# Performance work log

Hardware: AMD Instinct MI355X
Metric: run time of the kernel (lower is better)

Reference implementation:

```python
import jax, jax.numpy as jnp
import numpy as np

BATCH, N_MACS_PREV, CMS_PREV, NEUR_PREV = 256, 512, 8, 16
FILTER_LEN = 256
NUM_CMS, NUM_NEURONS = 32, 32
NUM_INPUTS = FILTER_LEN * CMS_PREV * NEUR_PREV  # 32768


def setup_inputs() -> dict:
    key = jax.random.key(0)
    k1, k2, k3 = jax.random.split(key, 3)
    x = jax.random.uniform(k1, (BATCH, N_MACS_PREV, CMS_PREV, NEUR_PREV), dtype=jnp.float32)
    input_filter = jax.random.randint(k2, (FILTER_LEN,), 0, N_MACS_PREV)
    # binary {0,1} weights, matching torch.randint(0, 2, ..., dtype=float32)
    weights = jax.random.randint(k3, (NUM_CMS, NUM_INPUTS, NUM_NEURONS), 0, 2).astype(jnp.float32)
    return {"x": x, "input_filter": input_filter, "weights": weights}


def reference(x, input_filter, weights):
    B = x.shape[0]
    # gather receptive field MACs and flatten: (B, num_inputs)
    xg = jnp.take(x, input_filter, axis=1).reshape(B, -1)
    # sum-normalize, nan_to_num handles all-zero rows (0/0 -> 0)
    xn = jnp.nan_to_num(xg / jnp.sum(xg, axis=-1, keepdims=True))
    # batched matmul: (B,I) x (C,I,N) -> (B,C,N)  (torch does (C,B,N) then permutes)
    acts = jnp.einsum('bi,cin->bcn', xn, weights)
    # familiarity-based softmax temperature
    familiarities = jnp.max(acts, axis=-1)          # (B, C)
    avg_fam = jnp.mean(familiarities)               # scalar
    softmax_temp = 1.0 / (avg_fam + 1e-4) - 1.0
    logits = acts / softmax_temp
    # categorical sample per (batch, cm); fixed key for determinism
    samples = jax.random.categorical(jax.random.key(42), logits, axis=-1)  # (B, C)
    # scatter one-hot write-out, int output as in torch
    out = jax.nn.one_hot(samples, NUM_NEURONS, dtype=jnp.int32)  # (B, C, N)
    return out
```

## Files before the change

kernel.cpp:

```cpp
#include <hip/hip_runtime.h>
#include <stdint.h>

#define BATCH 256
#define NMAC  512
#define ROWF  128
#define I_    32768
#define C_    32
#define N_    32
#define XROW  (NMAC * ROWF)

typedef float  f32x4  __attribute__((ext_vector_type(4)));
typedef __bf16 bf16x8 __attribute__((ext_vector_type(8)));

__device__ __forceinline__ uint32_t f2bf_rne(float f) {
    uint32_t u = __builtin_bit_cast(uint32_t, f);
    return (u + 0x7FFFu + ((u >> 16) & 1u)) >> 16;
}

__global__ __launch_bounds__(256) void k_sum(const float* __restrict__ x,
                                             const int* __restrict__ filt,
                                             float* __restrict__ S) {
    const int b = blockIdx.x;
    const int t = threadIdx.x;
    const float* xb = x + (size_t)b * XROW;
    float s = 0.f;
    for (int it = 0; it < 32; ++it) {
        int idx4 = it * 256 + t;
        int f = idx4 >> 5;
        int j4 = idx4 & 31;
        float4 v = *(const float4*)(xb + (size_t)filt[f] * ROWF + j4 * 4);
        s += v.x + v.y + v.z + v.w;
    }
    for (int o = 32; o > 0; o >>= 1) s += __shfl_down(s, o, 64);
    __shared__ float red[4];
    if ((t & 63) == 0) red[t >> 6] = s;
    __syncthreads();
    if (t == 0) S[b] = red[0] + red[1] + red[2] + red[3];
}

__global__ __launch_bounds__(256, 2) void k_gemm(const float* __restrict__ x,
                                                 const int* __restrict__ filt,
                                                 const float* __restrict__ w,
                                                 float* __restrict__ raw) {
    __shared__ __align__(16) unsigned short afr[32 * 512];
    __shared__ __align__(16) unsigned short wfr[8 * 512];

    const int t  = threadIdx.x;
    const int l  = t & 63;
    const int wv = t >> 6;
    const int chunk = blockIdx.x & 63;
    const int c0 = (blockIdx.x >> 6) * 4;

    f32x4 acc[4][8];
#pragma unroll
    for (int bt = 0; bt < 4; ++bt)
#pragma unroll
        for (int ct = 0; ct < 8; ++ct) acc[bt][ct] = f32x4{0.f, 0.f, 0.f, 0.f};

    const int ar     = t >> 3;
    const int ai     = t & 7;
    const int a_quad = ai >> 1;
    const int a_j    = (ai & 1) * 4;
    const int wn = t & 31;
    const int wc = t >> 5;

    for (int st = 0; st < 16; ++st) {
        const int ifull = chunk * 512 + st * 32;
        const int fidx  = filt[ifull >> 7];
        const int ioff  = ifull & 127;
        const float* xs = x + (size_t)fidx * ROWF + ioff;

#pragma unroll
        for (int rr = 0; rr < 8; ++rr) {
            int row = rr * 32 + ar;
            float4 v = *(const float4*)(xs + (size_t)row * XROW + ai * 4);
            uint32_t u0 = __builtin_bit_cast(uint32_t, v.x);
            uint32_t u1 = __builtin_bit_cast(uint32_t, v.y);
            uint32_t u2 = __builtin_bit_cast(uint32_t, v.z);
            uint32_t u3 = __builtin_bit_cast(uint32_t, v.w);
            float l0 = v.x - __builtin_bit_cast(float, u0 & 0xFFFF0000u);
            float l1 = v.y - __builtin_bit_cast(float, u1 & 0xFFFF0000u);
            float l2 = v.z - __builtin_bit_cast(float, u2 & 0xFFFF0000u);
            float l3 = v.w - __builtin_bit_cast(float, u3 & 0xFFFF0000u);
            uint2 hp, lp;
            hp.x = (u0 >> 16) | (u1 & 0xFFFF0000u);
            hp.y = (u2 >> 16) | (u3 & 0xFFFF0000u);
            lp.x = f2bf_rne(l0) | (f2bf_rne(l1) << 16);
            lp.y = f2bf_rne(l2) | (f2bf_rne(l3) << 16);
            int rt   = row >> 4;
            int lane = a_quad * 16 + (row & 15);
            int base = (rt * 2) * 512 + lane * 8 + a_j;
            *(uint2*)&afr[base]       = hp;
            *(uint2*)&afr[base + 512] = lp;
        }

#pragma unroll
        for (int q = 0; q < 8; ++q) {
            int sl  = wc + 8 * q;
            int c   = sl >> 4;
            int il  = (sl & 15) * 2;
            const float* wp = w + ((size_t)(c0 + c) * I_ + ifull + il) * N_ + wn;
            uint32_t u0 = __builtin_bit_cast(uint32_t, wp[0]);
            uint32_t u1 = __builtin_bit_cast(uint32_t, wp[N_]);
            uint32_t pk = (u0 >> 16) | (u1 & 0xFFFF0000u);
            int lane = (il >> 3) * 16 + (wn & 15);
            int ct   = c * 2 + (wn >> 4);
            *(uint32_t*)&wfr[ct * 512 + lane * 8 + (il & 7)] = pk;
        }
        __syncthreads();

        bf16x8 av[4][2];
#pragma unroll
        for (int bt = 0; bt < 4; ++bt)
#pragma unroll
            for (int p = 0; p < 2; ++p)
                av[bt][p] = *(const bf16x8*)&afr[((wv * 4 + bt) * 2 + p) * 512 + l * 8];
        bf16x8 bv[8];
#pragma unroll
        for (int ct = 0; ct < 8; ++ct)
            bv[ct] = *(const bf16x8*)&wfr[ct * 512 + l * 8];
#pragma unroll
        for (int bt = 0; bt < 4; ++bt)
#pragma unroll
            for (int ct = 0; ct < 8; ++ct) {
                acc[bt][ct] = __builtin_amdgcn_mfma_f32_16x16x32_bf16(av[bt][0], bv[ct], acc[bt][ct], 0, 0, 0);
                acc[bt][ct] = __builtin_amdgcn_mfma_f32_16x16x32_bf16(av[bt][1], bv[ct], acc[bt][ct], 0, 0, 0);
            }
        __syncthreads();
    }

    const int quad = l >> 4, n15 = l & 15;
#pragma unroll
    for (int bt = 0; bt < 4; ++bt) {
#pragma unroll
        for (int ct = 0; ct < 8; ++ct) {
            int c = c0 + (ct >> 1);
            int n = (ct & 1) * 16 + n15;
#pragma unroll
            for (int r = 0; r < 4; ++r) {
                int b = (wv * 4 + bt) * 16 + quad * 4 + r;
                atomicAdd(&raw[((size_t)b * C_ + c) * N_ + n], acc[bt][ct][r]);
            }
        }
    }
}

__global__ __launch_bounds__(256) void k_fam(const float* __restrict__ raw,
                                             const float* __restrict__ S,
                                             float* __restrict__ fam) {
    int r = blockIdx.x * 256 + threadIdx.x;
    const float4* ap = (const float4*)(raw + (size_t)r * N_);
    float m = -3.0e38f;
#pragma unroll
    for (int q = 0; q < 8; ++q) {
        float4 v = ap[q];
        m = fmaxf(m, fmaxf(fmaxf(v.x, v.y), fmaxf(v.z, v.w)));
    }
    m = m / S[r >> 5];
    for (int o = 32; o > 0; o >>= 1) m += __shfl_down(m, o, 64);
    __shared__ float red[4];
    if ((threadIdx.x & 63) == 0) red[threadIdx.x >> 6] = m;
    __syncthreads();
    if (threadIdx.x == 0) atomicAdd(fam, red[0] + red[1] + red[2] + red[3]);
}

__device__ __forceinline__ uint32_t rotl32(uint32_t x, uint32_t r) {
    return (x << r) | (x >> (32u - r));
}
__device__ __forceinline__ void threefry(uint32_t k0, uint32_t k1,
                                         uint32_t x0, uint32_t x1,
                                         uint32_t& o0, uint32_t& o1) {
    uint32_t ks2 = k0 ^ k1 ^ 0x1BD11BDAu;
    x0 += k0; x1 += k1;
    x0 += x1; x1 = rotl32(x1, 13); x1 ^= x0;
    x0 += x1; x1 = rotl32(x1, 15); x1 ^= x0;
    x0 += x1; x1 = rotl32(x1, 26); x1 ^= x0;
    x0 += x1; x1 = rotl32(x1, 6);  x1 ^= x0;
    x0 += k1; x1 += ks2 + 1u;
    x0 += x1; x1 = rotl32(x1, 17); x1 ^= x0;
    x0 += x1; x1 = rotl32(x1, 29); x1 ^= x0;
    x0 += x1; x1 = rotl32(x1, 16); x1 ^= x0;
    x0 += x1; x1 = rotl32(x1, 24); x1 ^= x0;
    x0 += ks2; x1 += k0 + 2u;
    x0 += x1; x1 = rotl32(x1, 13); x1 ^= x0;
    x0 += x1; x1 = rotl32(x1, 15); x1 ^= x0;
    x0 += x1; x1 = rotl32(x1, 26); x1 ^= x0;
    x0 += x1; x1 = rotl32(x1, 6);  x1 ^= x0;
    x0 += k0; x1 += k1 + 3u;
    x0 += x1; x1 = rotl32(x1, 17); x1 ^= x0;
    x0 += x1; x1 = rotl32(x1, 29); x1 ^= x0;
    x0 += x1; x1 = rotl32(x1, 16); x1 ^= x0;
    x0 += x1; x1 = rotl32(x1, 24); x1 ^= x0;
    x0 += k1; x1 += ks2 + 4u;
    x0 += x1; x1 = rotl32(x1, 13); x1 ^= x0;
    x0 += x1; x1 = rotl32(x1, 15); x1 ^= x0;
    x0 += x1; x1 = rotl32(x1, 26); x1 ^= x0;
    x0 += x1; x1 = rotl32(x1, 6);  x1 ^= x0;
    x0 += ks2; x1 += k0 + 5u;
    o0 = x0; o1 = x1;
}

__device__ __forceinline__ float gumbel_of(uint32_t bits) {
    uint32_t fb = (bits >> 9) | 0x3F800000u;
    float f = __builtin_bit_cast(float, fb) - 1.0f;
    float u = f + 1.17549435e-38f;
    return -logf(-logf(u));
}

__global__ __launch_bounds__(256) void k_sample(const float* __restrict__ raw,
                                                const float* __restrict__ S,
                                                const float* __restrict__ fam,
                                                int* __restrict__ out) {
    int r0 = blockIdx.x * 256 + threadIdx.x;
    int r1 = r0 + 4096;
    float avg  = fam[0] * (1.0f / 8192.0f);
    float temp = 1.0f / (avg + 1e-4f) - 1.0f;
    float sA = S[r0 >> 5], sB = S[r1 >> 5];
    const float* apA = raw + (size_t)r0 * N_;
    const float* apB = raw + (size_t)r1 * N_;

    float bestA = -3.4e38f, bestB = -3.4e38f;
    int biA = 0, biB = 0;
    for (int n = 0; n < 32; ++n) {
        uint32_t iA = (uint32_t)(r0 * 32 + n);
        uint32_t iB = (uint32_t)(r1 * 32 + n);
        uint32_t a0, a1, b0, b1;
        threefry(0u, 42u, 0u, iA, a0, a1);
        threefry(0u, 42u, 0u, iB, b0, b1);
        float vA = (apA[n] / sA) / temp + gumbel_of(a0 ^ a1);
        float vB = (apB[n] / sB) / temp + gumbel_of(b0 ^ b1);
        if (vA > bestA) { bestA = vA; biA = n; }
        if (vB > bestB) { bestB = vB; biB = n; }
    }
    int4* opA = (int4*)(out + (size_t)r0 * N_);
    int4* opB = (int4*)(out + (size_t)r1 * N_);
#pragma unroll
    for (int q = 0; q < 8; ++q) {
        int4 a, b;
        a.x = (q * 4 + 0) == biA; a.y = (q * 4 + 1) == biA;
        a.z = (q * 4 + 2) == biA; a.w = (q * 4 + 3) == biA;
        b.x = (q * 4 + 0) == biB; b.y = (q * 4 + 1) == biB;
        b.z = (q * 4 + 2) == biB; b.w = (q * 4 + 3) == biB;
        opA[q] = a; opB[q] = b;
    }
}

extern "C" void kernel_launch(void* const* d_in, const int* in_sizes, int n_in,
                              void* d_out, int out_size, void* d_ws, size_t ws_size,
                              hipStream_t stream) {
    const float* x    = (const float*)d_in[0];
    const int*   filt = (const int*)d_in[1];
    const float* w    = (const float*)d_in[2];
    int* out = (int*)d_out;

    char* ws = (char*)d_ws;
    float* raw = (float*)ws;
    float* fam = (float*)(ws + (1 << 20));
    float* S   = (float*)(ws + (1 << 20) + 128);

    hipMemsetAsync(ws, 0, (1 << 20) + 128, stream);
    hipLaunchKernelGGL(k_sum,    dim3(256), dim3(256), 0, stream, x, filt, S);
    hipLaunchKernelGGL(k_gemm,   dim3(512), dim3(256), 0, stream, x, filt, w, raw);
    hipLaunchKernelGGL(k_fam,    dim3(32),  dim3(256), 0, stream, raw, S, fam);
    hipLaunchKernelGGL(k_sample, dim3(16),  dim3(256), 0, stream, raw, S, fam, out);
}
```

Measured before the change: 305.8 us.

## Double-buffer GEMM loads, widen blocks to 512 threads, swizzle LDS, replace atomics with partial reduction

The split-K GEMM kernel now uses 512 threads per block, with each wave owning two row tiles. Global loads for the next K-step are prefetched into registers while the current step runs its MFMAs, and an XOR swizzle is applied to the LDS fragment layout to reduce bank conflicts. When the workspace is large enough, per-chunk partial results are written with plain stores and summed by a new reduction kernel, replacing the float atomics. This adds 64 partial buffers of traffic (about 32 MB) and one extra launch, and it raises register pressure from the prefetch buffers.

New measurement: 390.8 us. 1.28x slower.

```diff
diff --git a/kernel.cpp b/kernel.cpp
--- a/kernel.cpp
+++ b/kernel.cpp
@@ -8,6 +8,8 @@
 #define C_    32
 #define N_    32
 #define XROW  (NMAC * ROWF)
+#define NCH   64
+#define NST   16
 
 typedef float  f32x4  __attribute__((ext_vector_type(4)));
 typedef __bf16 bf16x8 __attribute__((ext_vector_type(8)));
@@ -38,10 +40,12 @@
     if (t == 0) S[b] = red[0] + red[1] + red[2] + red[3];
 }
 
-__global__ __launch_bounds__(256, 2) void k_gemm(const float* __restrict__ x,
+__global__ __launch_bounds__(512, 4) void k_gemm(const float* __restrict__ x,
                                                  const int* __restrict__ filt,
                                                  const float* __restrict__ w,
-                                                 float* __restrict__ raw) {
+                                                 float* __restrict__ part,
+                                                 float* __restrict__ raw,
+                                                 int use_part) {
     __shared__ __align__(16) unsigned short afr[32 * 512];
     __shared__ __align__(16) unsigned short wfr[8 * 512];
 
@@ -51,29 +55,68 @@
     const int chunk = blockIdx.x & 63;
     const int c0 = (blockIdx.x >> 6) * 4;
 
-    f32x4 acc[4][8];
-#pragma unroll
-    for (int bt = 0; bt < 4; ++bt)
-#pragma unroll
-        for (int ct = 0; ct < 8; ++ct) acc[bt][ct] = f32x4{0.f, 0.f, 0.f, 0.f};
-
-    const int ar     = t >> 3;
-    const int ai     = t & 7;
-    const int a_quad = ai >> 1;
-    const int a_j    = (ai & 1) * 4;
-    const int wn = t & 31;
-    const int wc = t >> 5;
-
-    for (int st = 0; st < 16; ++st) {
+    const int arow = t >> 1;
+    const int akq  = t & 1;
+    const int r15  = arow & 15;
+    const int rt_a = arow >> 4;
+    const float* xr = x + (size_t)arow * XROW + akq * 4;
+
+    const int wn  = t & 31;
+    const int wsl = t >> 5;
+
+    f32x4 acc0[8], acc1[8];
+#pragma unroll
+    for (int i = 0; i < 8; ++i) {
+        acc0[i] = f32x4{0.f, 0.f, 0.f, 0.f};
+        acc1[i] = f32x4{0.f, 0.f, 0.f, 0.f};
+    }
+
+    auto loadA = [&](int st, float4* A) {
         const int ifull = chunk * 512 + st * 32;
         const int fidx  = filt[ifull >> 7];
-        const int ioff  = ifull & 127;
-        const float* xs = x + (size_t)fidx * ROWF + ioff;
-
-#pragma unroll
-        for (int rr = 0; rr < 8; ++rr) {
-            int row = rr * 32 + ar;
-            float4 v = *(const float4*)(xs + (size_t)row * XROW + ai * 4);
+        const float* pa = xr + (size_t)fidx * ROWF + (ifull & 127);
+#pragma unroll
+        for (int jj = 0; jj < 4; ++jj)
+            A[jj] = *(const float4*)(pa + jj * 8);
+    };
+
+    auto loadW = [&](int st, uint2* W) {
+        const int ifull = chunk * 512 + st * 32;
+#pragma unroll
+        for (int q = 0; q < 2; ++q) {
+            int sl = wsl + 16 * q;
+            int c  = sl >> 3;
+            int kk = (sl & 7) * 4;
+            const float* wp = w + ((size_t)(c0 + c) * I_ + ifull + kk) * N_ + wn;
+            uint32_t u0 = __builtin_bit_cast(uint32_t, wp[0]);
+            uint32_t u1 = __builtin_bit_cast(uint32_t, wp[N_]);
+            uint32_t u2 = __builtin_bit_cast(uint32_t, wp[2 * N_]);
+            uint32_t u3 = __builtin_bit_cast(uint32_t, wp[3 * N_]);
+            W[q].x = (u0 >> 16) | (u1 & 0xFFFF0000u);
+            W[q].y = (u2 >> 16) | (u3 & 0xFFFF0000u);
+        }
+    };
+
+    auto storeW = [&](const uint2* W) {
+#pragma unroll
+        for (int q = 0; q < 2; ++q) {
+            int sl = wsl + 16 * q;
+            int c  = sl >> 3;
+            int kk = (sl & 7) * 4;
+            int L  = ((kk >> 3) << 4) + (wn & 15);
+            int P  = L ^ ((L >> 3) & 7);
+            int ct = c * 2 + (wn >> 4);
+            *(uint2*)&wfr[ct * 512 + P * 8 + (kk & 4)] = W[q];
+        }
+    };
+
+    auto storeA = [&](const float4* A) {
+#pragma unroll
+        for (int jj = 0; jj < 4; ++jj) {
+            float4 v = A[jj];
+            int k0 = (akq + 2 * jj) * 4;
+            int L  = ((k0 >> 3) << 4) + r15;
+            int P  = L ^ ((L >> 3) & 7);
             uint32_t u0 = __builtin_bit_cast(uint32_t, v.x);
             uint32_t u1 = __builtin_bit_cast(uint32_t, v.y);
             uint32_t u2 = __builtin_bit_cast(uint32_t, v.z);
@@ -87,62 +130,73 @@
             hp.y = (u2 >> 16) | (u3 & 0xFFFF0000u);
             lp.x = f2bf_rne(l0) | (f2bf_rne(l1) << 16);
             lp.y = f2bf_rne(l2) | (f2bf_rne(l3) << 16);
-            int rt   = row >> 4;
-            int lane = a_quad * 16 + (row & 15);
-            int base = (rt * 2) * 512 + lane * 8 + a_j;
+            int base = (rt_a * 2) * 512 + P * 8 + (k0 & 4);
             *(uint2*)&afr[base]       = hp;
             *(uint2*)&afr[base + 512] = lp;
         }
-
-#pragma unroll
-        for (int q = 0; q < 8; ++q) {
-            int sl  = wc + 8 * q;
-            int c   = sl >> 4;
-            int il  = (sl & 15) * 2;
-            const float* wp = w + ((size_t)(c0 + c) * I_ + ifull + il) * N_ + wn;
-            uint32_t u0 = __builtin_bit_cast(uint32_t, wp[0]);
-            uint32_t u1 = __builtin_bit_cast(uint32_t, wp[N_]);
-            uint32_t pk = (u0 >> 16) | (u1 & 0xFFFF0000u);
-            int lane = (il >> 3) * 16 + (wn & 15);
-            int ct   = c * 2 + (wn >> 4);
-            *(uint32_t*)&wfr[ct * 512 + lane * 8 + (il & 7)] = pk;
-        }
+    };
+
+    const int Pl8 = (l ^ ((l >> 3) & 7)) * 8;
+    auto MM = [&]() {
+        const int rt0 = wv * 2, rt1 = rt0 + 1;
+        bf16x8 a00 = *(const bf16x8*)&afr[(rt0 * 2 + 0) * 512 + Pl8];
+        bf16x8 a01 = *(const bf16x8*)&afr[(rt0 * 2 + 1) * 512 + Pl8];
+        bf16x8 a10 = *(const bf16x8*)&afr[(rt1 * 2 + 0) * 512 + Pl8];
+        bf16x8 a11 = *(const bf16x8*)&afr[(rt1 * 2 + 1) * 512 + Pl8];
+#pragma unroll
+        for (int i = 0; i < 8; ++i) {
+            bf16x8 b = *(const bf16x8*)&wfr[i * 512 + Pl8];
+            acc0[i] = __builtin_amdgcn_mfma_f32_16x16x32_bf16(a00, b, acc0[i], 0, 0, 0);
+            acc0[i] = __builtin_amdgcn_mfma_f32_16x16x32_bf16(a01, b, acc0[i], 0, 0, 0);
+            acc1[i] = __builtin_amdgcn_mfma_f32_16x16x32_bf16(a10, b, acc1[i], 0, 0, 0);
+            acc1[i] = __builtin_amdgcn_mfma_f32_16x16x32_bf16(a11, b, acc1[i], 0, 0, 0);
+        }
+    };
+
+    float4 Aa[4], Ab[4];
+    uint2  Wa[2], Wb[2];
+    loadA(0, Aa); loadW(0, Wa);
+    for (int st = 0; st < NST; st += 2) {
+        if (st) __syncthreads();
+        storeA(Aa); storeW(Wa);
+        loadA(st + 1, Ab); loadW(st + 1, Wb);
         __syncthreads();
-
-        bf16x8 av[4][2];
-#pragma unroll
-        for (int bt = 0; bt < 4; ++bt)
-#pragma unroll
-            for (int p = 0; p < 2; ++p)
-                av[bt][p] = *(const bf16x8*)&afr[((wv * 4 + bt) * 2 + p) * 512 + l * 8];
-        bf16x8 bv[8];
-#pragma unroll
-        for (int ct = 0; ct < 8; ++ct)
-            bv[ct] = *(const bf16x8*)&wfr[ct * 512 + l * 8];
-#pragma unroll
-        for (int bt = 0; bt < 4; ++bt)
-#pragma unroll
-            for (int ct = 0; ct < 8; ++ct) {
-                acc[bt][ct] = __builtin_amdgcn_mfma_f32_16x16x32_bf16(av[bt][0], bv[ct], acc[bt][ct], 0, 0, 0);
-                acc[bt][ct] = __builtin_amdgcn_mfma_f32_16x16x32_bf16(av[bt][1], bv[ct], acc[bt][ct], 0, 0, 0);
+        MM();
+        __syncthreads();
+        storeA(Ab); storeW(Wb);
+        if (st + 2 < NST) { loadA(st + 2, Aa); loadW(st + 2, Wa); }
+        __syncthreads();
+        MM();
+    }
+
+    const int quad = l >> 4, n15 = l & 15;
+    float* dst = use_part ? (part + (size_t)chunk * (BATCH * C_ * N_)) : raw;
+#pragma unroll
+    for (int rr = 0; rr < 2; ++rr) {
+        const f32x4* ac = rr ? acc1 : acc0;
+        const int bbase = (wv * 2 + rr) * 16 + quad * 4;
+#pragma unroll
+        for (int i = 0; i < 8; ++i) {
+            int c = c0 + (i >> 1);
+            int n = (i & 1) * 16 + n15;
+#pragma unroll
+            for (int r = 0; r < 4; ++r) {
+                size_t idx = ((size_t)(bbase + r) * C_ + c) * N_ + n;
+                if (use_part) dst[idx] = ac[i][r];
+                else          atomicAdd(&dst[idx], ac[i][r]);
             }
-        __syncthreads();
-    }
-
-    const int quad = l >> 4, n15 = l & 15;
-#pragma unroll
-    for (int bt = 0; bt < 4; ++bt) {
-#pragma unroll
-        for (int ct = 0; ct < 8; ++ct) {
-            int c = c0 + (ct >> 1);
-            int n = (ct & 1) * 16 + n15;
-#pragma unroll
-            for (int r = 0; r < 4; ++r) {
-                int b = (wv * 4 + bt) * 16 + quad * 4 + r;
-                atomicAdd(&raw[((size_t)b * C_ + c) * N_ + n], acc[bt][ct][r]);
-            }
-        }
-    }
+        }
+    }
+}
+
+__global__ __launch_bounds__(256) void k_reduce(const float* __restrict__ part,
+                                                float* __restrict__ raw) {
+    const int i4 = blockIdx.x * 256 + threadIdx.x;
+    const f32x4* p = (const f32x4*)part;
+    f32x4 s = f32x4{0.f, 0.f, 0.f, 0.f};
+#pragma unroll 8
+    for (int ch = 0; ch < NCH; ++ch) s += p[(size_t)ch * 65536 + i4];
+    ((f32x4*)raw)[i4] = s;
 }
 
 __global__ __launch_bounds__(256) void k_fam(const float* __restrict__ raw,
@@ -254,13 +308,23 @@
     int* out = (int*)d_out;
 
     char* ws = (char*)d_ws;
-    float* raw = (float*)ws;
-    float* fam = (float*)(ws + (1 << 20));
-    float* S   = (float*)(ws + (1 << 20) + 128);
-
-    hipMemsetAsync(ws, 0, (1 << 20) + 128, stream);
+    float* raw  = (float*)ws;
+    float* fam  = (float*)(ws + (1 << 20));
+    float* S    = (float*)(ws + (1 << 20) + 128);
+    float* part = (float*)(ws + (2u << 20));
+
+    const size_t need = (2u << 20) + (size_t)NCH * (BATCH * C_ * N_) * sizeof(float);
+    const int use_part = (ws_size >= need) ? 1 : 0;
+
+    if (use_part) {
+        hipMemsetAsync(ws + (1 << 20), 0, 128, stream);
+    } else {
+        hipMemsetAsync(ws, 0, (1 << 20) + 128, stream);
+    }
     hipLaunchKernelGGL(k_sum,    dim3(256), dim3(256), 0, stream, x, filt, S);
-    hipLaunchKernelGGL(k_gemm,   dim3(512), dim3(256), 0, stream, x, filt, w, raw);
+    hipLaunchKernelGGL(k_gemm,   dim3(512), dim3(512), 0, stream, x, filt, w, part, raw, use_part);
+    if (use_part)
+        hipLaunchKernelGGL(k_reduce, dim3(256), dim3(256), 0, stream, part, raw);
     hipLaunchKernelGGL(k_fam,    dim3(32),  dim3(256), 0, stream, raw, S, fam);
     hipLaunchKernelGGL(k_sample, dim3(16),  dim3(256), 0, stream, raw, S, fam, out);
 }
```

## Replace GEMM split-K atomics with partial buffers and a fused reduce kernel

Applied to the files above, without the earlier changes.

Each split-K chunk of the GEMM now writes its partial (B,C,N) tile to its own slice of a workspace buffer instead of issuing float atomicAdds into a shared output. A new reduce kernel sums the 64 partials, writes the raw activations, and computes the familiarity max and global sum, replacing the separate k_fam kernel. The goal is to remove heavy atomic contention (64 adds per output element). The cost is about 64 MB of extra global writes and reads. The new path runs only when the workspace holds at least about 66 MB; otherwise the old atomic path is used.

Result: faster. 280.7 us (-8.2%).

```diff
diff --git a/kernel.cpp b/kernel.cpp
--- a/kernel.cpp
+++ b/kernel.cpp
@@ -8,6 +8,7 @@
 #define C_    32
 #define N_    32
 #define XROW  (NMAC * ROWF)
+#define NCH   64
 
 typedef float  f32x4  __attribute__((ext_vector_type(4)));
 typedef __bf16 bf16x8 __attribute__((ext_vector_type(8)));
@@ -41,7 +42,9 @@
 __global__ __launch_bounds__(256, 2) void k_gemm(const float* __restrict__ x,
                                                  const int* __restrict__ filt,
                                                  const float* __restrict__ w,
-                                                 float* __restrict__ raw) {
+                                                 float* __restrict__ part,
+                                                 float* __restrict__ raw,
+                                                 int use_part) {
     __shared__ __align__(16) unsigned short afr[32 * 512];
     __shared__ __align__(16) unsigned short wfr[8 * 512];
 
@@ -130,19 +133,59 @@
     }
 
     const int quad = l >> 4, n15 = l & 15;
-#pragma unroll
-    for (int bt = 0; bt < 4; ++bt) {
-#pragma unroll
-        for (int ct = 0; ct < 8; ++ct) {
-            int c = c0 + (ct >> 1);
-            int n = (ct & 1) * 16 + n15;
-#pragma unroll
-            for (int r = 0; r < 4; ++r) {
-                int b = (wv * 4 + bt) * 16 + quad * 4 + r;
-                atomicAdd(&raw[((size_t)b * C_ + c) * N_ + n], acc[bt][ct][r]);
+    if (use_part) {
+        float* dst = part + (size_t)chunk * (BATCH * C_ * N_);
+#pragma unroll
+        for (int bt = 0; bt < 4; ++bt) {
+#pragma unroll
+            for (int ct = 0; ct < 8; ++ct) {
+                int c = c0 + (ct >> 1);
+                int n = (ct & 1) * 16 + n15;
+#pragma unroll
+                for (int r = 0; r < 4; ++r) {
+                    int b = (wv * 4 + bt) * 16 + quad * 4 + r;
+                    dst[((size_t)b * C_ + c) * N_ + n] = acc[bt][ct][r];
+                }
             }
         }
-    }
+    } else {
+#pragma unroll
+        for (int bt = 0; bt < 4; ++bt) {
+#pragma unroll
+            for (int ct = 0; ct < 8; ++ct) {
+                int c = c0 + (ct >> 1);
+                int n = (ct & 1) * 16 + n15;
+#pragma unroll
+                for (int r = 0; r < 4; ++r) {
+                    int b = (wv * 4 + bt) * 16 + quad * 4 + r;
+                    atomicAdd(&raw[((size_t)b * C_ + c) * N_ + n], acc[bt][ct][r]);
+                }
+            }
+        }
+    }
+}
+
+__global__ __launch_bounds__(256) void k_reduce(const float* __restrict__ part,
+                                                const float* __restrict__ S,
+                                                float* __restrict__ raw,
+                                                float* __restrict__ fam) {
+    const int i4 = blockIdx.x * 256 + threadIdx.x;
+    const f32x4* p = (const f32x4*)part;
+    f32x4 s = f32x4{0.f, 0.f, 0.f, 0.f};
+#pragma unroll 8
+    for (int ch = 0; ch < NCH; ++ch) s += p[(size_t)ch * 65536 + i4];
+    ((f32x4*)raw)[i4] = s;
+    float m = fmaxf(fmaxf(s[0], s[1]), fmaxf(s[2], s[3]));
+    m = fmaxf(m, __shfl_xor(m, 1, 64));
+    m = fmaxf(m, __shfl_xor(m, 2, 64));
+    m = fmaxf(m, __shfl_xor(m, 4, 64));
+    int r = i4 >> 3;
+    float v = ((i4 & 7) == 0) ? (m / S[r >> 5]) : 0.f;
+    for (int o = 32; o > 0; o >>= 1) v += __shfl_down(v, o, 64);
+    __shared__ float red[4];
+    if ((threadIdx.x & 63) == 0) red[threadIdx.x >> 6] = v;
+    __syncthreads();
+    if (threadIdx.x == 0) atomicAdd(fam, red[0] + red[1] + red[2] + red[3]);
 }
 
 __global__ __launch_bounds__(256) void k_fam(const float* __restrict__ raw,
@@ -254,13 +297,25 @@
     int* out = (int*)d_out;
 
     char* ws = (char*)d_ws;
-    float* raw = (float*)ws;
-    float* fam = (float*)(ws + (1 << 20));
-    float* S   = (float*)(ws + (1 << 20) + 128);
-
-    hipMemsetAsync(ws, 0, (1 << 20) + 128, stream);
-    hipLaunchKernelGGL(k_sum,    dim3(256), dim3(256), 0, stream, x, filt, S);
-    hipLaunchKernelGGL(k_gemm,   dim3(512), dim3(256), 0, stream, x, filt, w, raw);
-    hipLaunchKernelGGL(k_fam,    dim3(32),  dim3(256), 0, stream, raw, S, fam);
-    hipLaunchKernelGGL(k_sample, dim3(16),  dim3(256), 0, stream, raw, S, fam, out);
-}
+    float* raw  = (float*)ws;
+    float* fam  = (float*)(ws + (1 << 20));
+    float* S    = (float*)(ws + (1 << 20) + 128);
+    float* part = (float*)(ws + (2u << 20));
+
+    const size_t need = (2u << 20) + (size_t)NCH * (BATCH * C_ * N_) * sizeof(float);
+    const int use_part = (ws_size >= need) ? 1 : 0;
+
+    if (use_part) {
+        hipMemsetAsync(ws + (1 << 20), 0, 128, stream);
+        hipLaunchKernelGGL(k_sum,    dim3(256), dim3(256), 0, stream, x, filt, S);
+        hipLaunchKernelGGL(k_gemm,   dim3(512), dim3(256), 0, stream, x, filt, w, part, raw, 1);
+        hipLaunchKernelGGL(k_reduce, dim3(256), dim3(256), 0, stream, part, S, raw, fam);
+        hipLaunchKernelGGL(k_sample, dim3(16),  dim3(256), 0, stream, raw, S, fam, out);
+    } else {
+        hipMemsetAsync(ws, 0, (1 << 20) + 128, stream);
+        hipLaunchKernelGGL(k_sum,    dim3(256), dim3(256), 0, stream, x, filt, S);
+        hipLaunchKernelGGL(k_gemm,   dim3(512), dim3(256), 0, stream, x, filt, w, part, raw, 0);
+        hipLaunchKernelGGL(k_fam,    dim3(32),  dim3(256), 0, stream, raw, S, fam);
+        hipLaunchKernelGGL(k_sample, dim3(16),  dim3(256), 0, stream, raw, S, fam, out);
+    }
+}
```
